# Kernel tuning notes

Measured on AMD Instinct MI355X. Metric: run time of the kernel, lower is better.

The kernel has to match this reference:

```python
import jax, jax.numpy as jnp
import numpy as np

ROWS, COLS, NFEAT = 128, 128, 256
BATCH = 4096


def setup_inputs() -> dict:
    key = jax.random.key(0)
    k1, k2 = jax.random.split(key)
    xb = jax.random.normal(k1, (BATCH, NFEAT), dtype=jnp.float32)
    weights = jax.random.normal(k2, (ROWS, COLS, NFEAT), dtype=jnp.float32)
    return {"xb": xb, "weights": weights}


def reference(xb, weights):
    # Flatten codebook: (M, F) with M = rows*cols
    w = weights.reshape(-1, NFEAT)
    # Pairwise Euclidean distances via ||a||^2 + ||b||^2 - 2 a.b (single GEMM)
    a2 = jnp.sum(xb * xb, axis=-1, keepdims=True)            # (B, 1)
    b2 = jnp.sum(w * w, axis=-1)                             # (M,)
    d2 = a2 + b2[None, :] - 2.0 * jnp.einsum('bf,mf->bm', xb, w)  # (B, M)
    distances = jnp.sqrt(jnp.maximum(d2, 0.0))
    # BMU: argmin over codebook, converted to 2D map indices
    min_idxs = jnp.argmin(distances, axis=-1)                # (B,)
    bmus = jnp.stack([min_idxs // COLS, min_idxs % COLS], axis=-1)  # (B, 2)
    return bmus
```

## Files before the change

### kernel.cpp

```cpp
#include <hip/hip_runtime.h>
#include <cfloat>

#define NFEAT 256
#define BATCH 4096
#define MTOT  16384
#define NSTRIP 16
#define UMARGIN 0.75f

typedef __attribute__((ext_vector_type(8))) short bf16x8;
typedef __attribute__((ext_vector_type(4))) float f32x4;

__device__ __forceinline__ unsigned bf16pack(float a, float b) {
    unsigned ua = __float_as_uint(a), ub = __float_as_uint(b);
    unsigned ra = (ua + 0x7fffu + ((ua >> 16) & 1u)) >> 16;
    unsigned rb = (ub + 0x7fffu + ((ub >> 16) & 1u)) >> 16;
    return ra | (rb << 16);
}

__global__ __launch_bounds__(256) void prep_kernel(const float* __restrict__ src,
                                                   uint2* __restrict__ dstbf,
                                                   float* __restrict__ norm, int nrows) {
    int gid  = blockIdx.x * blockDim.x + threadIdx.x;
    int row  = gid >> 6;
    int lane = threadIdx.x & 63;
    if (row >= nrows) return;
    float4 v = *reinterpret_cast<const float4*>(src + (size_t)row * NFEAT + 4 * lane);
    dstbf[(size_t)row * 64 + lane] = make_uint2(bf16pack(v.x, v.y), bf16pack(v.z, v.w));
    float s = v.x * v.x + v.y * v.y + v.z * v.z + v.w * v.w;
    #pragma unroll
    for (int off = 32; off > 0; off >>= 1) s += __shfl_down(s, off);
    if (lane == 0) norm[row] = s;
}

__global__ __launch_bounds__(256, 2) void som_mfma_kernel(
        const unsigned short* __restrict__ Abf, const unsigned short* __restrict__ Bbf,
        const float* __restrict__ b2, float2* __restrict__ part) {
    __shared__ char smem[32768];

    const int t = threadIdx.x, l = t & 63;
    const int wid = t >> 6, wr = wid >> 1, wc = wid & 1;

    int bid = blockIdx.x;
    int xcd = bid & 7, cc = bid >> 3;
    int strip  = xcd * 2 + (cc >> 5);
    int m_tile = cc & 31;
    const int m0  = m_tile * 128;
    const int ns0 = strip * 1024;

    const int srow = (((t & 7) ^ ((t >> 3) & 7)) << 4);
    const char* pA = (const char*)Abf + (size_t)(m0 + (t >> 3)) * 512 + srow;
    const char* pB = (const char*)Bbf + (size_t)(ns0 + (t >> 3)) * 512 + srow;
    char* ldsA = smem + t * 16;
    char* ldsB = smem + 16384 + t * 16;

    float r0[4][4], r1[4][4];
    #pragma unroll
    for (int m = 0; m < 4; ++m)
        #pragma unroll
        for (int j = 0; j < 4; ++j) { r0[m][j] = -FLT_MAX; r1[m][j] = -FLT_MAX; }

    const unsigned mask = 0xFFFFFFE0u;

    for (int nt = 0; nt < 8; ++nt) {
        const int colbase = ns0 + nt * 128 + wc * 64 + (l & 15);
        float b2h[4];
        #pragma unroll
        for (int n = 0; n < 4; ++n) b2h[n] = -0.5f * b2[colbase + 16 * n];
        f32x4 acc[4][4];
        #pragma unroll
        for (int m = 0; m < 4; ++m)
            #pragma unroll
            for (int n = 0; n < 4; ++n)
                acc[m][n] = (f32x4){b2h[n], b2h[n], b2h[n], b2h[n]};

        #pragma unroll
        for (int kt = 0; kt < 4; ++kt) {
            __syncthreads();
            #pragma unroll
            for (int i = 0; i < 4; ++i) {
                __builtin_amdgcn_global_load_lds(
                    (const __attribute__((address_space(1))) void*)(pA + i * 16384 + kt * 128),
                    (__attribute__((address_space(3))) void*)(ldsA + i * 4096), 16, 0, 0);
                __builtin_amdgcn_global_load_lds(
                    (const __attribute__((address_space(1))) void*)(pB + (size_t)nt * 65536 + i * 16384 + kt * 128),
                    (__attribute__((address_space(3))) void*)(ldsB + i * 4096), 16, 0, 0);
            }
            __syncthreads();

            #pragma unroll
            for (int kk = 0; kk < 2; ++kk) {
                const int swz = (kk * 64 + (l >> 4) * 16) ^ ((l & 7) << 4);
                bf16x8 af[4], bfr[4];
                #pragma unroll
                for (int m = 0; m < 4; ++m) {
                    int row_l = wr * 64 + 16 * m + (l & 15);
                    af[m] = *(const bf16x8*)(smem + row_l * 128 + swz);
                }
                #pragma unroll
                for (int n = 0; n < 4; ++n) {
                    int col_l = wc * 64 + 16 * n + (l & 15);
                    bfr[n] = *(const bf16x8*)(smem + 16384 + col_l * 128 + swz);
                }
                #pragma unroll
                for (int m = 0; m < 4; ++m)
                    #pragma unroll
                    for (int n = 0; n < 4; ++n)
                        acc[m][n] = __builtin_amdgcn_mfma_f32_16x16x32_bf16(
                            af[m], bfr[n], acc[m][n], 0, 0, 0);
            }
        }

        #pragma unroll
        for (int n = 0; n < 4; ++n) {
            const unsigned idn = (unsigned)(nt * 4 + n);
            #pragma unroll
            for (int m = 0; m < 4; ++m) {
                #pragma unroll
                for (int j = 0; j < 4; ++j) {
                    float p = __uint_as_float((__float_as_uint(acc[m][n][j]) & mask) | idn);
                    float nr1 = __builtin_amdgcn_fmed3f(r0[m][j], r1[m][j], p);
                    r0[m][j] = fmaxf(r0[m][j], p);
                    r1[m][j] = nr1;
                }
            }
        }
    }

    const int slot = wc * 16 + (l & 15);
    #pragma unroll
    for (int m = 0; m < 4; ++m)
        #pragma unroll
        for (int j = 0; j < 4; ++j) {
            int rowg = m0 + wr * 64 + 16 * m + (l >> 4) * 4 + j;
            part[((size_t)rowg * NSTRIP + strip) * 32 + slot] =
                make_float2(r0[m][j], r1[m][j]);
        }
}

__global__ __launch_bounds__(256) void refine_kernel(
        const float* __restrict__ xb, const float* __restrict__ w,
        const float* __restrict__ a2, const float* __restrict__ b2,
        const float* __restrict__ part, int* __restrict__ out) {
    __shared__ float sumax[4];
    __shared__ unsigned long long skey[4];
    const int row = blockIdx.x, t = threadIdx.x;

    const float4 v4 = ((const float4*)(part + (size_t)row * 1024))[t];
    float um = fmaxf(fmaxf(v4.x, v4.y), fmaxf(v4.z, v4.w));
    #pragma unroll
    for (int off = 32; off > 0; off >>= 1) um = fmaxf(um, __shfl_xor(um, off));
    if ((t & 63) == 0) sumax[t >> 6] = um;
    __syncthreads();
    um = fmaxf(fmaxf(sumax[0], sumax[1]), fmaxf(sumax[2], sumax[3]));
    const float cut = um - UMARGIN;

    const float a2r = a2[row];
    const float4* xr = (const float4*)(xb + (size_t)row * NFEAT);
    float uq[4] = {v4.x, v4.y, v4.z, v4.w};
    unsigned long long key = ~0ull;
    #pragma unroll
    for (int q = 0; q < 4; ++q) {
        if (uq[q] >= cut) {
            int f = 4 * t + q;
            unsigned low5 = __float_as_uint(uq[q]) & 31u;
            int st   = f >> 6;
            int slot = (f >> 1) & 31;
            int col  = st * 1024 + (int)(low5 >> 2) * 128 + (slot >> 4) * 64
                     + (int)(low5 & 3) * 16 + (slot & 15);
            const float4* wr_ = (const float4*)(w + (size_t)col * NFEAT);
            float dot = 0.f;
            #pragma unroll 8
            for (int k = 0; k < NFEAT / 4; ++k) {
                float4 xv = xr[k], wv = wr_[k];
                dot += xv.x * wv.x + xv.y * wv.y + xv.z * wv.z + xv.w * wv.w;
            }
            float d2 = a2r + b2[col] - 2.f * dot;
            float s  = sqrtf(fmaxf(d2, 0.f));
            unsigned long long kk =
                ((unsigned long long)__float_as_uint(s) << 32) | (unsigned)col;
            key = kk < key ? kk : key;
        }
    }
    #pragma unroll
    for (int off = 32; off > 0; off >>= 1) {
        unsigned long long o = __shfl_xor(key, off);
        key = o < key ? o : key;
    }
    if ((t & 63) == 0) skey[t >> 6] = key;
    __syncthreads();
    if (t == 0) {
        unsigned long long k = skey[0];
        #pragma unroll
        for (int i = 1; i < 4; ++i) k = skey[i] < k ? skey[i] : k;
        int idx = (int)(k & 0xffffffffu);
        out[2 * row]     = idx >> 7;
        out[2 * row + 1] = idx & 127;
    }
}

extern "C" void kernel_launch(void* const* d_in, const int* in_sizes, int n_in,
                              void* d_out, int out_size, void* d_ws, size_t ws_size,
                              hipStream_t stream) {
    const float* xb = (const float*)d_in[0];
    const float* w  = (const float*)d_in[1];
    int* out = (int*)d_out;

    char* ws = (char*)d_ws;
    unsigned short* Abf = (unsigned short*)ws;
    unsigned short* Bbf = (unsigned short*)(ws + (2u << 20));
    float* a2   = (float*)(ws + (10u << 20));
    float* b2   = (float*)(ws + (10u << 20) + (64u << 10));
    float* part = (float*)(ws + (10u << 20) + (128u << 10));

    prep_kernel<<<(MTOT * 64) / 256, 256, 0, stream>>>(w, (uint2*)Bbf, b2, MTOT);
    prep_kernel<<<(BATCH * 64) / 256, 256, 0, stream>>>(xb, (uint2*)Abf, a2, BATCH);

    som_mfma_kernel<<<512, 256, 0, stream>>>(Abf, Bbf, b2, (float2*)part);

    refine_kernel<<<BATCH, 256, 0, stream>>>(xb, w, a2, b2, part, out);
}
```

Baseline: 72.83 us.

## Restructure MFMA argmax with resident A tile, double-buffered B, in-block top-2 reduction

```diff
diff --git a/kernel.cpp b/kernel.cpp
--- a/kernel.cpp
+++ b/kernel.cpp
@@ -4,11 +4,16 @@
 #define NFEAT 256
 #define BATCH 4096
 #define MTOT  16384
-#define NSTRIP 16
+#define NSTRIP 8
+#define STRIPW 2048
+#define NHALF 32
 #define UMARGIN 0.75f
 
 typedef __attribute__((ext_vector_type(8))) short bf16x8;
 typedef __attribute__((ext_vector_type(4))) float f32x4;
+
+#define GP(p)    ((const __attribute__((address_space(1))) void*)(p))
+#define LDSP(p)  ((__attribute__((address_space(3))) void*)(p))
 
 __device__ __forceinline__ unsigned bf16pack(float a, float b) {
     unsigned ua = __float_as_uint(a), ub = __float_as_uint(b);
@@ -17,182 +22,208 @@
     return ra | (rb << 16);
 }
 
-__global__ __launch_bounds__(256) void prep_kernel(const float* __restrict__ src,
-                                                   uint2* __restrict__ dstbf,
-                                                   float* __restrict__ norm, int nrows) {
+__global__ __launch_bounds__(256) void prep_kernel(const float* __restrict__ xb,
+                                                   const float* __restrict__ w,
+                                                   uint2* __restrict__ Abf,
+                                                   uint2* __restrict__ Bbf,
+                                                   float* __restrict__ a2,
+                                                   float* __restrict__ b2) {
     int gid  = blockIdx.x * blockDim.x + threadIdx.x;
     int row  = gid >> 6;
-    int lane = threadIdx.x & 63;
-    if (row >= nrows) return;
-    float4 v = *reinterpret_cast<const float4*>(src + (size_t)row * NFEAT + 4 * lane);
-    dstbf[(size_t)row * 64 + lane] = make_uint2(bf16pack(v.x, v.y), bf16pack(v.z, v.w));
+    int lane = gid & 63;
+    const float* src;
+    uint2* dst;
+    float* nrm;
+    if (row < MTOT) {
+        src = w + (size_t)row * NFEAT;  dst = Bbf + (size_t)row * 64;  nrm = b2 + row;
+    } else {
+        int r = row - MTOT;
+        src = xb + (size_t)r * NFEAT;   dst = Abf + (size_t)r * 64;    nrm = a2 + r;
+    }
+    float4 v = ((const float4*)src)[lane];
+    dst[lane] = make_uint2(bf16pack(v.x, v.y), bf16pack(v.z, v.w));
     float s = v.x * v.x + v.y * v.y + v.z * v.z + v.w * v.w;
     #pragma unroll
     for (int off = 32; off > 0; off >>= 1) s += __shfl_down(s, off);
-    if (lane == 0) norm[row] = s;
-}
-
-__global__ __launch_bounds__(256, 2) void som_mfma_kernel(
+    if (lane == 0) *nrm = s;
+}
+
+__global__ __launch_bounds__(512, 1) void som_mfma_kernel(
         const unsigned short* __restrict__ Abf, const unsigned short* __restrict__ Bbf,
-        const float* __restrict__ b2, float2* __restrict__ part) {
-    __shared__ char smem[32768];
+        const float* __restrict__ b2, float* __restrict__ part) {
+    __shared__ char smem[139264];
 
     const int t = threadIdx.x, l = t & 63;
-    const int wid = t >> 6, wr = wid >> 1, wc = wid & 1;
-
-    int bid = blockIdx.x;
-    int xcd = bid & 7, cc = bid >> 3;
-    int strip  = xcd * 2 + (cc >> 5);
-    int m_tile = cc & 31;
-    const int m0  = m_tile * 128;
-    const int ns0 = strip * 1024;
-
-    const int srow = (((t & 7) ^ ((t >> 3) & 7)) << 4);
-    const char* pA = (const char*)Abf + (size_t)(m0 + (t >> 3)) * 512 + srow;
-    const char* pB = (const char*)Bbf + (size_t)(ns0 + (t >> 3)) * 512 + srow;
-    char* ldsA = smem + t * 16;
-    char* ldsB = smem + 16384 + t * 16;
-
-    float r0[4][4], r1[4][4];
-    #pragma unroll
-    for (int m = 0; m < 4; ++m)
+    const int wid = t >> 6, wm = wid >> 1, wc = wid & 1;
+    const int strip = blockIdx.x & 7;
+    const int m0 = (blockIdx.x >> 3) * 128;
+    const int ns0 = strip * STRIPW;
+
+    const int rowt = t >> 5;
+    const int swzcol = ((t & 31) << 4) ^ ((rowt & 7) << 4);
+    const char* gA = (const char*)Abf + (size_t)(m0 + rowt) * 512 + swzcol;
+    const char* gB = (const char*)Bbf + (size_t)(ns0 + rowt) * 512 + swzcol;
+
+    #pragma unroll
+    for (int i = 0; i < 8; ++i)
+        __builtin_amdgcn_global_load_lds(GP(gA + i * 8192), LDSP(smem + t * 16 + i * 8192), 16, 0, 0);
+    __builtin_amdgcn_global_load_lds(GP((const char*)b2 + (size_t)ns0 * 4 + t * 16),
+                                     LDSP(smem + 131072 + t * 16), 16, 0, 0);
+    #pragma unroll
+    for (int i = 0; i < 4; ++i)
+        __builtin_amdgcn_global_load_lds(GP(gB + i * 8192), LDSP(smem + 65536 + t * 16 + i * 8192), 16, 0, 0);
+    #pragma unroll
+    for (int i = 0; i < 4; ++i)
+        __builtin_amdgcn_global_load_lds(GP(gB + 32768 + i * 8192), LDSP(smem + 98304 + t * 16 + i * 8192), 16, 0, 0);
+
+    float r0[2][4], r1[2][4];
+    #pragma unroll
+    for (int m = 0; m < 2; ++m)
         #pragma unroll
         for (int j = 0; j < 4; ++j) { r0[m][j] = -FLT_MAX; r1[m][j] = -FLT_MAX; }
 
-    const unsigned mask = 0xFFFFFFE0u;
-
-    for (int nt = 0; nt < 8; ++nt) {
-        const int colbase = ns0 + nt * 128 + wc * 64 + (l & 15);
-        float b2h[4];
-        #pragma unroll
-        for (int n = 0; n < 4; ++n) b2h[n] = -0.5f * b2[colbase + 16 * n];
-        f32x4 acc[4][4];
-        #pragma unroll
-        for (int m = 0; m < 4; ++m)
+    for (int h = 0; h < NHALF; ++h) {
+        if (h < NHALF - 2) asm volatile("s_waitcnt vmcnt(4)" ::: "memory");
+        else               asm volatile("s_waitcnt vmcnt(0)" ::: "memory");
+        __builtin_amdgcn_s_barrier();
+        asm volatile("" ::: "memory");
+
+        const char* bufB = smem + 65536 + ((h & 1) << 15);
+        const int cl = h * 64 + wc * 32 + (l & 15);
+        const float b20 = -0.5f * *(const float*)(smem + 131072 + cl * 4);
+        const float b21 = -0.5f * *(const float*)(smem + 131072 + cl * 4 + 64);
+
+        f32x4 acc[2][2];
+        #pragma unroll
+        for (int m = 0; m < 2; ++m) {
+            acc[m][0] = (f32x4){b20, b20, b20, b20};
+            acc[m][1] = (f32x4){b21, b21, b21, b21};
+        }
+
+        #pragma unroll
+        for (int kk = 0; kk < 8; ++kk) {
+            const int swz = (kk * 64 + (l >> 4) * 16) ^ ((l & 7) << 4);
+            bf16x8 af0 = *(const bf16x8*)(smem + (wm * 32 + (l & 15)) * 512 + swz);
+            bf16x8 af1 = *(const bf16x8*)(smem + (wm * 32 + 16 + (l & 15)) * 512 + swz);
+            bf16x8 bf0 = *(const bf16x8*)(bufB + (wc * 32 + (l & 15)) * 512 + swz);
+            bf16x8 bf1 = *(const bf16x8*)(bufB + (wc * 32 + 16 + (l & 15)) * 512 + swz);
+            acc[0][0] = __builtin_amdgcn_mfma_f32_16x16x32_bf16(af0, bf0, acc[0][0], 0, 0, 0);
+            acc[0][1] = __builtin_amdgcn_mfma_f32_16x16x32_bf16(af0, bf1, acc[0][1], 0, 0, 0);
+            acc[1][0] = __builtin_amdgcn_mfma_f32_16x16x32_bf16(af1, bf0, acc[1][0], 0, 0, 0);
+            acc[1][1] = __builtin_amdgcn_mfma_f32_16x16x32_bf16(af1, bf1, acc[1][1], 0, 0, 0);
+        }
+
+        #pragma unroll
+        for (int n = 0; n < 2; ++n) {
+            const unsigned idn = (unsigned)(h * 2 + n);
             #pragma unroll
-            for (int n = 0; n < 4; ++n)
-                acc[m][n] = (f32x4){b2h[n], b2h[n], b2h[n], b2h[n]};
-
-        #pragma unroll
-        for (int kt = 0; kt < 4; ++kt) {
-            __syncthreads();
-            #pragma unroll
-            for (int i = 0; i < 4; ++i) {
-                __builtin_amdgcn_global_load_lds(
-                    (const __attribute__((address_space(1))) void*)(pA + i * 16384 + kt * 128),
-                    (__attribute__((address_space(3))) void*)(ldsA + i * 4096), 16, 0, 0);
-                __builtin_amdgcn_global_load_lds(
-                    (const __attribute__((address_space(1))) void*)(pB + (size_t)nt * 65536 + i * 16384 + kt * 128),
-                    (__attribute__((address_space(3))) void*)(ldsB + i * 4096), 16, 0, 0);
-            }
-            __syncthreads();
-
-            #pragma unroll
-            for (int kk = 0; kk < 2; ++kk) {
-                const int swz = (kk * 64 + (l >> 4) * 16) ^ ((l & 7) << 4);
-                bf16x8 af[4], bfr[4];
-                #pragma unroll
-                for (int m = 0; m < 4; ++m) {
-                    int row_l = wr * 64 + 16 * m + (l & 15);
-                    af[m] = *(const bf16x8*)(smem + row_l * 128 + swz);
-                }
-                #pragma unroll
-                for (int n = 0; n < 4; ++n) {
-                    int col_l = wc * 64 + 16 * n + (l & 15);
-                    bfr[n] = *(const bf16x8*)(smem + 16384 + col_l * 128 + swz);
-                }
-                #pragma unroll
-                for (int m = 0; m < 4; ++m)
-                    #pragma unroll
-                    for (int n = 0; n < 4; ++n)
-                        acc[m][n] = __builtin_amdgcn_mfma_f32_16x16x32_bf16(
-                            af[m], bfr[n], acc[m][n], 0, 0, 0);
-            }
-        }
-
-        #pragma unroll
-        for (int n = 0; n < 4; ++n) {
-            const unsigned idn = (unsigned)(nt * 4 + n);
-            #pragma unroll
-            for (int m = 0; m < 4; ++m) {
+            for (int m = 0; m < 2; ++m)
                 #pragma unroll
                 for (int j = 0; j < 4; ++j) {
-                    float p = __uint_as_float((__float_as_uint(acc[m][n][j]) & mask) | idn);
+                    float p = __uint_as_float((__float_as_uint(acc[m][n][j]) & 0xFFFFFFC0u) | idn);
                     float nr1 = __builtin_amdgcn_fmed3f(r0[m][j], r1[m][j], p);
                     r0[m][j] = fmaxf(r0[m][j], p);
                     r1[m][j] = nr1;
                 }
+        }
+
+        asm volatile("" ::: "memory");
+        __builtin_amdgcn_s_barrier();
+        asm volatile("" ::: "memory");
+        if (h + 2 < NHALF) {
+            const char* gBn = gB + (size_t)(h + 2) * 32768;
+            const int dstb = 65536 + ((h & 1) << 15);
+            #pragma unroll
+            for (int i = 0; i < 4; ++i)
+                __builtin_amdgcn_global_load_lds(GP(gBn + i * 8192),
+                                                 LDSP(smem + dstb + t * 16 + i * 8192), 16, 0, 0);
+        }
+    }
+
+    asm volatile("" ::: "memory");
+    __builtin_amdgcn_s_barrier();
+    asm volatile("" ::: "memory");
+    float* sm = (float*)smem;
+    #pragma unroll
+    for (int m = 0; m < 2; ++m)
+        #pragma unroll
+        for (int j = 0; j < 4; ++j) {
+            unsigned u0 = __float_as_uint(r0[m][j]);
+            unsigned u1 = __float_as_uint(r1[m][j]);
+            u0 = (u0 & 0xFFFFF800u) | ((u0 & 63u) << 5) | ((unsigned)wc << 4) | (unsigned)(l & 15);
+            u1 = (u1 & 0xFFFFF800u) | ((u1 & 63u) << 5) | ((unsigned)wc << 4) | (unsigned)(l & 15);
+            float v0 = __uint_as_float(u0), v1 = __uint_as_float(u1);
+            #pragma unroll
+            for (int off = 1; off < 16; off <<= 1) {
+                float o0 = __shfl_xor(v0, off), o1 = __shfl_xor(v1, off);
+                float nv1 = fmaxf(fminf(v0, o0), fmaxf(v1, o1));
+                v0 = fmaxf(v0, o0);
+                v1 = nv1;
             }
-        }
-    }
-
-    const int slot = wc * 16 + (l & 15);
-    #pragma unroll
-    for (int m = 0; m < 4; ++m)
-        #pragma unroll
-        for (int j = 0; j < 4; ++j) {
-            int rowg = m0 + wr * 64 + 16 * m + (l >> 4) * 4 + j;
-            part[((size_t)rowg * NSTRIP + strip) * 32 + slot] =
-                make_float2(r0[m][j], r1[m][j]);
-        }
+            if ((l & 15) == 0) {
+                int row_l = wm * 32 + m * 16 + (l >> 4) * 4 + j;
+                sm[row_l * 4 + wc * 2 + 0] = v0;
+                sm[row_l * 4 + wc * 2 + 1] = v1;
+            }
+        }
+    asm volatile("" ::: "memory");
+    __builtin_amdgcn_s_barrier();
+    asm volatile("" ::: "memory");
+    if (t < 128) {
+        float a0 = sm[t * 4 + 0], a1 = sm[t * 4 + 1];
+        float c0 = sm[t * 4 + 2], c1 = sm[t * 4 + 3];
+        float v0 = fmaxf(a0, c0);
+        float v1 = fmaxf(fminf(a0, c0), fmaxf(a1, c1));
+        float2* pp = (float2*)(part + ((size_t)(m0 + t) * NSTRIP + strip) * 2);
+        *pp = make_float2(v0, v1);
+    }
 }
 
 __global__ __launch_bounds__(256) void refine_kernel(
         const float* __restrict__ xb, const float* __restrict__ w,
         const float* __restrict__ a2, const float* __restrict__ b2,
         const float* __restrict__ part, int* __restrict__ out) {
-    __shared__ float sumax[4];
-    __shared__ unsigned long long skey[4];
-    const int row = blockIdx.x, t = threadIdx.x;
-
-    const float4 v4 = ((const float4*)(part + (size_t)row * 1024))[t];
-    float um = fmaxf(fmaxf(v4.x, v4.y), fmaxf(v4.z, v4.w));
-    #pragma unroll
-    for (int off = 32; off > 0; off >>= 1) um = fmaxf(um, __shfl_xor(um, off));
-    if ((t & 63) == 0) sumax[t >> 6] = um;
-    __syncthreads();
-    um = fmaxf(fmaxf(sumax[0], sumax[1]), fmaxf(sumax[2], sumax[3]));
-    const float cut = um - UMARGIN;
-
-    const float a2r = a2[row];
-    const float4* xr = (const float4*)(xb + (size_t)row * NFEAT);
-    float uq[4] = {v4.x, v4.y, v4.z, v4.w};
+    const int t = threadIdx.x, l = t & 63;
+    const int row = blockIdx.x * 4 + (t >> 6);
+
+    const float* pr = part + (size_t)row * (NSTRIP * 2);
+    float v = (l < NSTRIP * 2) ? pr[l] : -FLT_MAX;
+    float mx = v;
+    #pragma unroll
+    for (int off = 1; off < 64; off <<= 1) mx = fmaxf(mx, __shfl_xor(mx, off));
+    const float cut = mx - UMARGIN;
+
     unsigned long long key = ~0ull;
-    #pragma unroll
-    for (int q = 0; q < 4; ++q) {
-        if (uq[q] >= cut) {
-            int f = 4 * t + q;
-            unsigned low5 = __float_as_uint(uq[q]) & 31u;
-            int st   = f >> 6;
-            int slot = (f >> 1) & 31;
-            int col  = st * 1024 + (int)(low5 >> 2) * 128 + (slot >> 4) * 64
-                     + (int)(low5 & 3) * 16 + (slot & 15);
-            const float4* wr_ = (const float4*)(w + (size_t)col * NFEAT);
-            float dot = 0.f;
-            #pragma unroll 8
-            for (int k = 0; k < NFEAT / 4; ++k) {
-                float4 xv = xr[k], wv = wr_[k];
-                dot += xv.x * wv.x + xv.y * wv.y + xv.z * wv.z + xv.w * wv.w;
-            }
-            float d2 = a2r + b2[col] - 2.f * dot;
-            float s  = sqrtf(fmaxf(d2, 0.f));
-            unsigned long long kk =
-                ((unsigned long long)__float_as_uint(s) << 32) | (unsigned)col;
-            key = kk < key ? kk : key;
-        }
-    }
-    #pragma unroll
-    for (int off = 32; off > 0; off >>= 1) {
+    if (l < NSTRIP * 2 && v >= cut) {
+        unsigned b = __float_as_uint(v);
+        int lane4 = b & 15, wcb = (b >> 4) & 1, hn = (b >> 5) & 63;
+        int col = (l >> 1) * STRIPW + (hn >> 1) * 64 + wcb * 32 + (hn & 1) * 16 + lane4;
+        const float4* xr = (const float4*)(xb + (size_t)row * NFEAT);
+        const float4* wr = (const float4*)(w + (size_t)col * NFEAT);
+        float s0 = 0.f, s1 = 0.f, s2 = 0.f, s3 = 0.f;
+        #pragma unroll
+        for (int k = 0; k < 16; ++k) {
+            float4 x0 = xr[4 * k + 0], w0 = wr[4 * k + 0];
+            float4 x1 = xr[4 * k + 1], w1 = wr[4 * k + 1];
+            float4 x2 = xr[4 * k + 2], w2 = wr[4 * k + 2];
+            float4 x3 = xr[4 * k + 3], w3 = wr[4 * k + 3];
+            s0 += x0.x * w0.x + x0.y * w0.y + x0.z * w0.z + x0.w * w0.w;
+            s1 += x1.x * w1.x + x1.y * w1.y + x1.z * w1.z + x1.w * w1.w;
+            s2 += x2.x * w2.x + x2.y * w2.y + x2.z * w2.z + x2.w * w2.w;
+            s3 += x3.x * w3.x + x3.y * w3.y + x3.z * w3.z + x3.w * w3.w;
+        }
+        float dot = (s0 + s1) + (s2 + s3);
+        float dd = a2[row] + b2[col] - 2.f * dot;
+        float s = sqrtf(fmaxf(dd, 0.f));
+        key = ((unsigned long long)__float_as_uint(s) << 32) | (unsigned)col;
+    }
+    #pragma unroll
+    for (int off = 1; off < 64; off <<= 1) {
         unsigned long long o = __shfl_xor(key, off);
         key = o < key ? o : key;
     }
-    if ((t & 63) == 0) skey[t >> 6] = key;
-    __syncthreads();
-    if (t == 0) {
-        unsigned long long k = skey[0];
-        #pragma unroll
-        for (int i = 1; i < 4; ++i) k = skey[i] < k ? skey[i] : k;
-        int idx = (int)(k & 0xffffffffu);
+    if (l == 0) {
+        int idx = (int)(key & 0xffffffffu);
         out[2 * row]     = idx >> 7;
         out[2 * row + 1] = idx & 127;
     }
@@ -212,10 +243,8 @@
     float* b2   = (float*)(ws + (10u << 20) + (64u << 10));
     float* part = (float*)(ws + (10u << 20) + (128u << 10));
 
-    prep_kernel<<<(MTOT * 64) / 256, 256, 0, stream>>>(w, (uint2*)Bbf, b2, MTOT);
-    prep_kernel<<<(BATCH * 64) / 256, 256, 0, stream>>>(xb, (uint2*)Abf, a2, BATCH);
-
-    som_mfma_kernel<<<512, 256, 0, stream>>>(Abf, Bbf, b2, (float2*)part);
-
-    refine_kernel<<<BATCH, 256, 0, stream>>>(xb, w, a2, b2, part, out);
-}
+    prep_kernel<<<((MTOT + BATCH) * 64) / 256, 256, 0, stream>>>(xb, w, (uint2*)Abf,
+                                                                 (uint2*)Bbf, a2, b2);
+    som_mfma_kernel<<<256, 512, 0, stream>>>(Abf, Bbf, b2, part);
+    refine_kernel<<<BATCH / 4, 256, 0, stream>>>(xb, w, a2, b2, part, out);
+}
```

Result: slower. 85.26 us (+17.1%).
